# Performance work log

Hardware: AMD Instinct MI355X
Metric: run time of the kernel (lower is better)

## Reference

```python
import jax, jax.numpy as jnp
import numpy as np

N, E, F_IN, D, D_OUT = 100000, 1600000, 64, 20, 16
EPS = 1e-5


def _mean_agg(x, src, dst, n):
    # gather source features, scatter-mean onto destination nodes
    s = jax.ops.segment_sum(x[src], dst, num_segments=n)
    cnt = jax.ops.segment_sum(jnp.ones((src.shape[0], 1), x.dtype), dst, num_segments=n)
    return s / jnp.maximum(cnt, 1.0)


def _batchnorm(h, g, b):
    mu = jnp.mean(h, axis=0)
    var = jnp.mean(jnp.square(h - mu), axis=0)  # biased variance, BatchNorm1d training math
    return (h - mu) * jax.lax.rsqrt(var + EPS) * g + b


def _block(x, src, dst, Wl, bl, Wr, Ws, bs, Wn, bn, g, be):
    # SAGEConv: lin_l(mean_agg) + lin_r(x); plus linskip; then lin, BN, ReLU
    agg = _mean_agg(x, src, dst, N)
    h = agg @ Wl + bl + x @ Wr + x @ Ws + bs
    h = h @ Wn + bn
    return jax.nn.relu(_batchnorm(h, g, be))


def setup_inputs() -> dict:
    key = jax.random.key(0)
    ks = jax.random.split(key, 32)
    sc = lambda fi: 1.0 / np.sqrt(fi)
    d = {}
    d["x"] = jax.random.normal(ks[0], (N, F_IN), jnp.float32)
    d["edge_index"] = jax.random.randint(ks[1], (2, E), 0, N, dtype=jnp.int64)
    d["edge_attr"] = jax.random.normal(ks[2], (E, 1), jnp.float32)
    # layer 1 (in = F_IN)
    d["Wl1"] = jax.random.normal(ks[3], (F_IN, D), jnp.float32) * sc(F_IN)
    d["bl1"] = jnp.zeros((D,), jnp.float32)
    d["Wr1"] = jax.random.normal(ks[4], (F_IN, D), jnp.float32) * sc(F_IN)
    d["Ws1"] = jax.random.normal(ks[5], (F_IN, D), jnp.float32) * sc(F_IN)
    d["bs1"] = jnp.zeros((D,), jnp.float32)
    d["Wn1"] = jax.random.normal(ks[6], (D, D), jnp.float32) * sc(D)
    d["bn1"] = jnp.zeros((D,), jnp.float32)
    d["g1"] = jnp.ones((D,), jnp.float32)
    d["be1"] = jnp.zeros((D,), jnp.float32)
    # layers 2-4 stacked (in = D)
    d["Wlm"] = jax.random.normal(ks[7], (3, D, D), jnp.float32) * sc(D)
    d["blm"] = jnp.zeros((3, D), jnp.float32)
    d["Wrm"] = jax.random.normal(ks[8], (3, D, D), jnp.float32) * sc(D)
    d["Wsm"] = jax.random.normal(ks[9], (3, D, D), jnp.float32) * sc(D)
    d["bsm"] = jnp.zeros((3, D), jnp.float32)
    d["Wnm"] = jax.random.normal(ks[10], (3, D, D), jnp.float32) * sc(D)
    d["bnm"] = jnp.zeros((3, D), jnp.float32)
    d["gm"] = jnp.ones((3, D), jnp.float32)
    d["bem"] = jnp.zeros((3, D), jnp.float32)
    # layer 5 (no BN/ReLU, out = D_OUT)
    d["Wl5"] = jax.random.normal(ks[11], (D, D), jnp.float32) * sc(D)
    d["bl5"] = jnp.zeros((D,), jnp.float32)
    d["Wr5"] = jax.random.normal(ks[12], (D, D), jnp.float32) * sc(D)
    d["Ws5"] = jax.random.normal(ks[13], (D, D), jnp.float32) * sc(D)
    d["bs5"] = jnp.zeros((D,), jnp.float32)
    d["Wn5"] = jax.random.normal(ks[14], (D, D_OUT), jnp.float32) * sc(D)
    d["bn5"] = jnp.zeros((D_OUT,), jnp.float32)
    return d


def reference(x, edge_index, edge_attr,
              Wl1, bl1, Wr1, Ws1, bs1, Wn1, bn1, g1, be1,
              Wlm, blm, Wrm, Wsm, bsm, Wnm, bnm, gm, bem,
              Wl5, bl5, Wr5, Ws5, bs5, Wn5, bn5):
    src, dst = edge_index[0], edge_index[1]
    # edge_attr is accepted by the torch forward but unused
    h = _block(x, src, dst, Wl1, bl1, Wr1, Ws1, bs1, Wn1, bn1, g1, be1)
    for i in range(3):  # layers 2-4
        h = _block(h, src, dst, Wlm[i], blm[i], Wrm[i], Wsm[i], bsm[i],
                   Wnm[i], bnm[i], gm[i], bem[i])
    # layer 5: sage + skip, final linear, no norm/relu
    agg = _mean_agg(h, src, dst, N)
    h = agg @ Wl5 + bl5 + h @ Wr5 + h @ Ws5 + bs5
    return h @ Wn5 + bn5
```

## Files before the change

kernel.cpp:

```cpp
#include <hip/hip_runtime.h>

constexpr int Nn   = 100000;
constexpr int Ne   = 1600000;
constexpr int FINN = 64;
constexpr int Dh   = 20;
constexpr int Dout = 16;
constexpr float EPSV = 1e-5f;

constexpr int NR  = 16;
constexpr int RSZ = Nn / NR;
constexpr int NSL = 32;
constexpr int P1B = 400;
constexpr int P1E = Ne / P1B;

constexpr size_t OFF_WC1  = 0;
constexpr size_t OFF_C1   = 2560;
constexpr size_t OFF_WCM  = 2592;
constexpr size_t OFF_CM   = 4992;
constexpr size_t OFF_WC5  = 5088;
constexpr size_t OFF_C5   = 5728;
constexpr size_t OFF_ST   = 5760;
constexpr size_t OFF_OFFS = 8192;
constexpr size_t OFF_BSUM = 208896;
constexpr size_t OFF_CNT  = 209408;
constexpr size_t OFF_CSR  = 309760;
constexpr size_t OFF_XA   = 1910784;
constexpr size_t OFF_XB   = 3510784;
constexpr size_t OFF_HP   = 5110784;
constexpr size_t OFF_BHT  = OFF_HP;
constexpr size_t OFF_OBHT = OFF_HP + 6400;
constexpr size_t OFF_RB   = OFF_HP + 12800;

__device__ inline unsigned short f2b(float x) {
    unsigned b = __float_as_uint(x);
    return (unsigned short)((b + 0x7FFFu + ((b >> 16) & 1u)) >> 16);
}
__device__ inline float b2f(unsigned short u) {
    return __uint_as_float(((unsigned)u) << 16);
}
__device__ inline float blo(unsigned u) { return __uint_as_float(u << 16); }
__device__ inline float bhi(unsigned u) { return __uint_as_float(u & 0xFFFF0000u); }
__device__ inline unsigned bpack(float lo, float hi) {
    return (unsigned)f2b(lo) | ((unsigned)f2b(hi) << 16);
}

__global__ void prep_weights(
    const float* __restrict__ Wl1, const float* __restrict__ bl1,
    const float* __restrict__ Wr1, const float* __restrict__ Ws1,
    const float* __restrict__ bs1, const float* __restrict__ Wn1,
    const float* __restrict__ bn1,
    const float* __restrict__ Wlm, const float* __restrict__ blm,
    const float* __restrict__ Wrm, const float* __restrict__ Wsm,
    const float* __restrict__ bsm, const float* __restrict__ Wnm,
    const float* __restrict__ bnm,
    const float* __restrict__ Wl5, const float* __restrict__ bl5,
    const float* __restrict__ Wr5, const float* __restrict__ Ws5,
    const float* __restrict__ bs5, const float* __restrict__ Wn5,
    const float* __restrict__ bn5,
    float* __restrict__ wc1, float* __restrict__ c1,
    float* __restrict__ wcm, float* __restrict__ cm,
    float* __restrict__ wc5, float* __restrict__ c5)
{
    int layer = blockIdx.x;
    int t = threadIdx.x;
    if (layer == 0) {
        for (int idx = t; idx < FINN * Dh; idx += blockDim.x) {
            int k = idx / Dh, j = idx % Dh;
            float a = 0.f, b = 0.f;
            for (int d = 0; d < Dh; ++d) {
                float wn = Wn1[d * Dh + j];
                a += Wl1[k * Dh + d] * wn;
                b += (Wr1[k * Dh + d] + Ws1[k * Dh + d]) * wn;
            }
            wc1[k * 40 + j] = a;
            wc1[k * 40 + 20 + j] = b;
        }
        for (int j = t; j < Dh; j += blockDim.x) {
            float c0 = 0.f;
            for (int d = 0; d < Dh; ++d) c0 += (bl1[d] + bs1[d]) * Wn1[d * Dh + j];
            c1[j] = c0 + bn1[j];
        }
    } else if (layer <= 3) {
        int i = layer - 1;
        const float* Wl = Wlm + i * Dh * Dh;
        const float* Wr = Wrm + i * Dh * Dh;
        const float* Ws = Wsm + i * Dh * Dh;
        const float* Wn = Wnm + i * Dh * Dh;
        const float* bl = blm + i * Dh;
        const float* bs = bsm + i * Dh;
        const float* bn = bnm + i * Dh;
        float* wc = wcm + i * 800;
        float* cc = cm + i * 32;
        for (int idx = t; idx < Dh * Dh; idx += blockDim.x) {
            int k = idx / Dh, j = idx % Dh;
            float a = 0.f, b = 0.f;
            for (int d = 0; d < Dh; ++d) {
                float wn = Wn[d * Dh + j];
                a += Wl[k * Dh + d] * wn;
                b += (Wr[k * Dh + d] + Ws[k * Dh + d]) * wn;
            }
            wc[k * 40 + j] = a;
            wc[k * 40 + 20 + j] = b;
        }
        for (int j = t; j < Dh; j += blockDim.x) {
            float c0 = 0.f;
            for (int d = 0; d < Dh; ++d) c0 += (bl[d] + bs[d]) * Wn[d * Dh + j];
            cc[j] = c0 + bn[j];
        }
    } else {
        for (int idx = t; idx < Dh * Dout; idx += blockDim.x) {
            int k = idx / Dout, j = idx % Dout;
            float a = 0.f, b = 0.f;
            for (int d = 0; d < Dh; ++d) {
                float wn = Wn5[d * Dout + j];
                a += Wl5[k * Dh + d] * wn;
                b += (Wr5[k * Dh + d] + Ws5[k * Dh + d]) * wn;
            }
            wc5[k * 32 + j] = a;
            wc5[k * 32 + 16 + j] = b;
        }
        for (int j = t; j < Dout; j += blockDim.x) {
            float c0 = 0.f;
            for (int d = 0; d < Dh; ++d) c0 += (bl5[d] + bs5[d]) * Wn5[d * Dout + j];
            c5[j] = c0 + bn5[j];
        }
    }
}

__global__ __launch_bounds__(256) void hist1(const int* __restrict__ dst, unsigned* __restrict__ bhT) {
    __shared__ unsigned h[16 * NR];
    int b = blockIdx.x, t = threadIdx.x;
    for (int i = t; i < 16 * NR; i += 256) h[i] = 0;
    __syncthreads();
    int sub = t & 15;
    int e0 = b * P1E, e1 = min(e0 + P1E, Ne);
    for (int e = e0 + t; e < e1; e += 256) {
        int r = dst[e] / RSZ;
        atomicAdd(&h[sub * NR + r], 1u);
    }
    __syncthreads();
    if (t < NR) {
        unsigned s = 0;
        for (int i = 0; i < 16; ++i) s += h[i * NR + t];
        bhT[t * P1B + b] = s;
    }
}

__global__ __launch_bounds__(1024) void scan1(
    const unsigned* __restrict__ bhT, unsigned* __restrict__ obhT, unsigned* __restrict__ rbase)
{
    __shared__ unsigned rtot[NR];
    int t = threadIdx.x;
    int w = t >> 6, lane = t & 63;
    constexpr int PER = (P1B + 63) / 64;
    if (w < NR) {
        unsigned v[PER];
        unsigned s = 0;
#pragma unroll
        for (int i = 0; i < PER; ++i) {
            int b = lane * PER + i;
            v[i] = (b < P1B) ? bhT[w * P1B + b] : 0u;
            s += v[i];
        }
        unsigned val = s;
        for (int off = 1; off < 64; off <<= 1) {
            unsigned u = __shfl_up(val, off, 64);
            if (lane >= off) val += u;
        }
        unsigned run = val - s;
#pragma unroll
        for (int i = 0; i < PER; ++i) {
            int b = lane * PER + i;
            if (b < P1B) obhT[w * P1B + b] = run;
            run += v[i];
        }
        if (lane == 63) rtot[w] = val;
    }
    __syncthreads();
    if (t == 0) {
        unsigned base = 0;
        for (int r = 0; r < NR; ++r) { rbase[r] = base; base += rtot[r]; }
        rbase[NR] = base;
    }
}

__global__ __launch_bounds__(256) void scatter1(
    const int* __restrict__ src, const int* __restrict__ dst,
    const unsigned* __restrict__ obhT, const unsigned* __restrict__ rbase,
    unsigned* __restrict__ ebuf)
{
    __shared__ unsigned cur[NR];
    int b = blockIdx.x, t = threadIdx.x;
    if (t < NR) cur[t] = rbase[t] + obhT[t * P1B + b];
    __syncthreads();
    int e0 = b * P1E, e1 = min(e0 + P1E, Ne);
    for (int e = e0 + t; e < e1; e += 256) {
        int d = dst[e];
        int r = d / RSZ;
        unsigned dl = (unsigned)(d - r * RSZ);
        unsigned pos = atomicAdd(&cur[r], 1u);
        ebuf[pos] = (dl << 17) | (unsigned)src[e];
    }
}

__global__ __launch_bounds__(256) void hist2(
    const unsigned* __restrict__ ebuf, const unsigned* __restrict__ rbase,
    unsigned short* __restrict__ part)
{
    __shared__ unsigned h[RSZ];
    int b = blockIdx.x, t = threadIdx.x;
    int r = b % NR, s = b / NR;
    for (int i = t; i < RSZ; i += 256) h[i] = 0;
    __syncthreads();
    unsigned lo = rbase[r], hi = rbase[r + 1];
    unsigned step = (hi - lo + NSL - 1) / NSL;
    unsigned e0 = lo + (unsigned)s * step;
    unsigned e1 = e0 + step; if (e1 > hi) e1 = hi;
    for (unsigned e = e0 + t; e < e1; e += 256)
        atomicAdd(&h[ebuf[e] >> 17], 1u);
    __syncthreads();
    unsigned short* p = part + (size_t)b * RSZ;
    for (int i = t; i < RSZ; i += 256) p[i] = (unsigned short)h[i];
}

__global__ void col_prefix(unsigned short* __restrict__ part, unsigned* __restrict__ cnt) {
    int d = blockIdx.x * blockDim.x + threadIdx.x;
    if (d >= Nn) return;
    int r = d / RSZ, dl = d - r * RSZ;
    unsigned run = 0;
#pragma unroll
    for (int s = 0; s < NSL; ++s) {
        size_t idx = ((size_t)s * NR + r) * RSZ + dl;
        unsigned v = part[idx];
        part[idx] = (unsigned short)run;
        run += v;
    }
    cnt[d] = run;
}

__global__ void scan_blocksums(const unsigned* __restrict__ cnt, unsigned* __restrict__ bsum, int n) {
    __shared__ unsigned sd[256];
    int b = blockIdx.x, t = threadIdx.x;
    int base = b * 1024;
    unsigned s = 0;
    for (int i = t; i < 1024; i += 256) {
        int idx = base + i;
        if (idx < n) s += cnt[idx];
    }
    sd[t] = s;
    __syncthreads();
    for (int off = 128; off > 0; off >>= 1) {
        if (t < off) sd[t] += sd[t + off];
        __syncthreads();
    }
    if (t == 0) bsum[b] = sd[0];
}

__global__ void scan_bsum(unsigned* __restrict__ bsum, int nb) {
    __shared__ unsigned sh[128];
    int t = threadIdx.x;
    unsigned v = (t < nb) ? bsum[t] : 0u;
    sh[t] = v;
    __syncthreads();
    for (int off = 1; off < 128; off <<= 1) {
        unsigned add = (t >= off) ? sh[t - off] : 0u;
        __syncthreads();
        sh[t] += add;
        __syncthreads();
    }
    if (t < nb) bsum[t] = sh[t] - v;
}

__global__ void scan_final(const unsigned* __restrict__ cnt, const unsigned* __restrict__ bsum,
                           unsigned* __restrict__ offs, int n) {
    __shared__ unsigned wsum[4], woff[4];
    int b = blockIdx.x, t = threadIdx.x;
    int base = b * 1024 + t * 4;
    unsigned v[4];
    unsigned s = 0;
#pragma unroll
    for (int i = 0; i < 4; ++i) {
        int idx = base + i;
        v[i] = (idx < n) ? cnt[idx] : 0u;
        s += v[i];
    }
    unsigned lane = t & 63;
    int w = t >> 6;
    unsigned val = s;
    for (int off = 1; off < 64; off <<= 1) {
        unsigned u = __shfl_up(val, off, 64);
        if (lane >= off) val += u;
    }
    if (lane == 63) wsum[w] = val;
    __syncthreads();
    if (t == 0) {
        unsigned r = 0;
        for (int i = 0; i < 4; ++i) { woff[i] = r; r += wsum[i]; }
    }
    __syncthreads();
    unsigned run = bsum[b] + woff[w] + (val - s);
#pragma unroll
    for (int i = 0; i < 4; ++i) {
        int idx = base + i;
        if (idx < n) {
            offs[idx] = run;
            run += v[i];
            if (idx == n - 1) offs[n] = run;
        }
    }
}

__global__ __launch_bounds__(256) void fill2(
    const unsigned* __restrict__ ebuf, const unsigned* __restrict__ rbase,
    const unsigned* __restrict__ offs, const unsigned short* __restrict__ part,
    unsigned* __restrict__ csr)
{
    __shared__ unsigned cur[RSZ];
    int b = blockIdx.x, t = threadIdx.x;
    int r = b % NR, s = b / NR;
    int lon = r * RSZ;
    const unsigned short* p = part + (size_t)b * RSZ;
    for (int i = t; i < RSZ; i += 256)
        cur[i] = offs[lon + i] + p[i];
    __syncthreads();
    unsigned lo = rbase[r], hi = rbase[r + 1];
    unsigned step = (hi - lo + NSL - 1) / NSL;
    unsigned e0 = lo + (unsigned)s * step;
    unsigned e1 = e0 + step; if (e1 > hi) e1 = hi;
    for (unsigned e = e0 + t; e < e1; e += 256) {
        unsigned v = ebuf[e];
        unsigned pos = atomicAdd(&cur[v >> 17], 1u);
        csr[pos] = v & 0x1FFFFu;
    }
}

template <int FINt, int FO, bool NORM, bool INBF16>
__global__ __launch_bounds__(256) void gemm_kernel(
    const void* __restrict__ xin_, const float* __restrict__ stats,
    const float* __restrict__ g, const float* __restrict__ be,
    const float* __restrict__ wc, const float* __restrict__ cvec,
    unsigned short* __restrict__ xa, unsigned short* __restrict__ xb)
{
    constexpr int XS  = ((FO + 7) / 8) * 8;
    constexpr int XSI = ((FINt + 7) / 8) * 8;
    __shared__ float sscale[Dh], sshift[Dh];
    int t = threadIdx.x;
    if (NORM) {
        if (t < Dh) {
            float mu = stats[t] * (1.0f / Nn);
            float var = stats[32 + t] * (1.0f / Nn) - mu * mu;
            float sc = g[t] * rsqrtf(var + EPSV);
            sscale[t] = sc;
            sshift[t] = be[t] - mu * sc;
        }
        __syncthreads();
    }
    int n = blockIdx.x * blockDim.x + t;
    if (n >= Nn) return;

    float acc[2 * FO];
#pragma unroll
    for (int j = 0; j < 2 * FO; ++j) acc[j] = 0.f;

#pragma unroll
    for (int c = 0; c < FINt / 4; ++c) {
        float xs[4];
        if (INBF16) {
            const unsigned short* xr = (const unsigned short*)xin_ + (size_t)n * XSI;
            ushort4 v = *(const ushort4*)(xr + 4 * c);
            xs[0] = b2f(v.x); xs[1] = b2f(v.y); xs[2] = b2f(v.z); xs[3] = b2f(v.w);
        } else {
            const float* xr = (const float*)xin_ + (size_t)n * FINt;
            float4 v = *(const float4*)(xr + 4 * c);
            xs[0] = v.x; xs[1] = v.y; xs[2] = v.z; xs[3] = v.w;
        }
        if (NORM) {
#pragma unroll
            for (int kk = 0; kk < 4; ++kk)
                xs[kk] = fmaxf(xs[kk] * sscale[4 * c + kk] + sshift[4 * c + kk], 0.0f);
        }
#pragma unroll
        for (int kk = 0; kk < 4; ++kk) {
            float xk = xs[kk];
            const float* wr = wc + (4 * c + kk) * (2 * FO);
#pragma unroll
            for (int j = 0; j < 2 * FO; ++j) acc[j] = fmaf(xk, wr[j], acc[j]);
        }
    }

    unsigned short* xao = xa + (size_t)n * XS;
    unsigned short* xbo = xb + (size_t)n * XS;
#pragma unroll
    for (int c = 0; c < FO / 4; ++c) {
        ushort4 o;
        o.x = f2b(acc[4 * c + 0]);
        o.y = f2b(acc[4 * c + 1]);
        o.z = f2b(acc[4 * c + 2]);
        o.w = f2b(acc[4 * c + 3]);
        *(ushort4*)(xao + 4 * c) = o;
        ushort4 p;
        p.x = f2b(acc[FO + 4 * c + 0] + cvec[4 * c + 0]);
        p.y = f2b(acc[FO + 4 * c + 1] + cvec[4 * c + 1]);
        p.z = f2b(acc[FO + 4 * c + 2] + cvec[4 * c + 2]);
        p.w = f2b(acc[FO + 4 * c + 3] + cvec[4 * c + 3]);
        *(ushort4*)(xbo + 4 * c) = p;
    }
}

template <int F, bool WITH_STATS, bool OUTBF16>
__global__ __launch_bounds__(256) void pull_kernel(
    const unsigned* __restrict__ offs, const unsigned* __restrict__ csr,
    const unsigned short* __restrict__ xa, const unsigned short* __restrict__ xb,
    void* __restrict__ out_, float* __restrict__ stats)
{
    constexpr int C  = (F + 7) / 8;
    constexpr int XS = C * 8;
    __shared__ float sstat[2 * F];
    int t = threadIdx.x;
    if (WITH_STATS) {
        if (t < 2 * F) sstat[t] = 0.f;
        __syncthreads();
    }
    int tid = blockIdx.x * blockDim.x + t;
    int n = tid / C;
    int c = tid % C;
    int valid = (c == C - 1) ? (F - 8 * (C - 1)) : 8;
    bool act = (n < Nn);
    float h[8];
    if (act) {
        unsigned b = offs[n], e = offs[n + 1];
        const unsigned short* base = xa + c * 8;
        float acc[8];
#pragma unroll
        for (int j = 0; j < 8; ++j) acc[j] = 0.f;
        unsigned k = b;
        for (; k + 8 <= e; k += 8) {
            unsigned s[8];
#pragma unroll
            for (int i = 0; i < 8; ++i) s[i] = csr[k + i];
            uint4 v[8];
#pragma unroll
            for (int i = 0; i < 8; ++i) v[i] = *(const uint4*)(base + (size_t)s[i] * XS);
#pragma unroll
            for (int i = 0; i < 8; ++i) {
                acc[0] += blo(v[i].x); acc[1] += bhi(v[i].x);
                acc[2] += blo(v[i].y); acc[3] += bhi(v[i].y);
                acc[4] += blo(v[i].z); acc[5] += bhi(v[i].z);
                acc[6] += blo(v[i].w); acc[7] += bhi(v[i].w);
            }
        }
        for (; k < e; ++k) {
            unsigned s0 = csr[k];
            uint4 v = *(const uint4*)(base + (size_t)s0 * XS);
            acc[0] += blo(v.x); acc[1] += bhi(v.x);
            acc[2] += blo(v.y); acc[3] += bhi(v.y);
            acc[4] += blo(v.z); acc[5] += bhi(v.z);
            acc[6] += blo(v.w); acc[7] += bhi(v.w);
        }
        float inv = 1.0f / fmaxf((float)(e - b), 1.0f);
        uint4 xv = *(const uint4*)(xb + (size_t)n * XS + c * 8);
        float xf[8] = { blo(xv.x), bhi(xv.x), blo(xv.y), bhi(xv.y),
                        blo(xv.z), bhi(xv.z), blo(xv.w), bhi(xv.w) };
#pragma unroll
        for (int j = 0; j < 8; ++j) h[j] = fmaf(acc[j], inv, xf[j]);
        if (OUTBF16) {
            unsigned short* o = (unsigned short*)out_ + (size_t)n * XS + c * 8;
            if (valid == 8) {
                uint4 w;
                w.x = bpack(h[0], h[1]); w.y = bpack(h[2], h[3]);
                w.z = bpack(h[4], h[5]); w.w = bpack(h[6], h[7]);
                *(uint4*)o = w;
            } else {
                ushort4 w4;
                w4.x = f2b(h[0]); w4.y = f2b(h[1]); w4.z = f2b(h[2]); w4.w = f2b(h[3]);
                *(ushort4*)o = w4;
            }
        } else {
            float* o = (float*)out_ + (size_t)n * F + c * 8;
            float4 v0; v0.x = h[0]; v0.y = h[1]; v0.z = h[2]; v0.w = h[3];
            *(float4*)o = v0;
            if (valid == 8) {
                float4 v1; v1.x = h[4]; v1.y = h[5]; v1.z = h[6]; v1.w = h[7];
                *(float4*)(o + 4) = v1;
            }
        }
    }
    if (WITH_STATS) {
        if (act) {
            for (int j = 0; j < valid; ++j) {
                atomicAdd(&sstat[c * 8 + j], h[j]);
                atomicAdd(&sstat[F + c * 8 + j], h[j] * h[j]);
            }
        }
        __syncthreads();
        if (t < F) {
            atomicAdd(&stats[t], sstat[t]);
        } else if (t < 2 * F) {
            atomicAdd(&stats[32 + (t - F)], sstat[t]);
        }
    }
}

extern "C" void kernel_launch(void* const* d_in, const int* in_sizes, int n_in,
                              void* d_out, int out_size, void* d_ws, size_t ws_size,
                              hipStream_t stream) {
    const float* x   = (const float*)d_in[0];
    const int* ei    = (const int*)d_in[1];
    const int* esrc  = ei;
    const int* edst  = ei + Ne;
    const float* Wl1 = (const float*)d_in[3];
    const float* bl1 = (const float*)d_in[4];
    const float* Wr1 = (const float*)d_in[5];
    const float* Ws1 = (const float*)d_in[6];
    const float* bs1 = (const float*)d_in[7];
    const float* Wn1 = (const float*)d_in[8];
    const float* bn1 = (const float*)d_in[9];
    const float* g1  = (const float*)d_in[10];
    const float* be1 = (const float*)d_in[11];
    const float* Wlm = (const float*)d_in[12];
    const float* blm = (const float*)d_in[13];
    const float* Wrm = (const float*)d_in[14];
    const float* Wsm = (const float*)d_in[15];
    const float* bsm = (const float*)d_in[16];
    const float* Wnm = (const float*)d_in[17];
    const float* bnm = (const float*)d_in[18];
    const float* gm  = (const float*)d_in[19];
    const float* bem = (const float*)d_in[20];
    const float* Wl5 = (const float*)d_in[21];
    const float* bl5 = (const float*)d_in[22];
    const float* Wr5 = (const float*)d_in[23];
    const float* Ws5 = (const float*)d_in[24];
    const float* bs5 = (const float*)d_in[25];
    const float* Wn5 = (const float*)d_in[26];
    const float* bn5 = (const float*)d_in[27];

    float* ws   = (float*)d_ws;
    unsigned* u = (unsigned*)d_ws;
    float* wc1   = ws + OFF_WC1;
    float* c1    = ws + OFF_C1;
    float* wcm   = ws + OFF_WCM;
    float* cm    = ws + OFF_CM;
    float* wc5   = ws + OFF_WC5;
    float* c5    = ws + OFF_C5;
    float* stats = ws + OFF_ST;
    unsigned* offs = u + OFF_OFFS;
    unsigned* bsum = u + OFF_BSUM;
    unsigned* cnt  = u + OFF_CNT;
    unsigned* csr  = u + OFF_CSR;
    unsigned short* xa = (unsigned short*)(ws + OFF_XA);
    unsigned* ebuf = u + OFF_XA;
    unsigned short* xb = (unsigned short*)(ws + OFF_XB);
    unsigned short* part = (unsigned short*)(ws + OFF_XB);
    unsigned short* hp = (unsigned short*)(ws + OFF_HP);
    unsigned* bhT  = u + OFF_BHT;
    unsigned* obhT = u + OFF_OBHT;
    unsigned* rbase = u + OFF_RB;

    hipMemsetAsync(stats, 0, 256 * sizeof(float), stream);

    prep_weights<<<5, 256, 0, stream>>>(Wl1, bl1, Wr1, Ws1, bs1, Wn1, bn1,
                                        Wlm, blm, Wrm, Wsm, bsm, Wnm, bnm,
                                        Wl5, bl5, Wr5, Ws5, bs5, Wn5, bn5,
                                        wc1, c1, wcm, cm, wc5, c5);

    hist1<<<P1B, 256, 0, stream>>>(edst, bhT);
    scan1<<<1, 1024, 0, stream>>>(bhT, obhT, rbase);
    scatter1<<<P1B, 256, 0, stream>>>(esrc, edst, obhT, rbase, ebuf);
    hist2<<<NR * NSL, 256, 0, stream>>>(ebuf, rbase, part);
    col_prefix<<<(Nn + 255) / 256, 256, 0, stream>>>(part, cnt);
    constexpr int NB = (Nn + 1023) / 1024;
    scan_blocksums<<<NB, 256, 0, stream>>>(cnt, bsum, Nn);
    scan_bsum<<<1, 128, 0, stream>>>(bsum, NB);
    scan_final<<<NB, 256, 0, stream>>>(cnt, bsum, offs, Nn);
    fill2<<<NR * NSL, 256, 0, stream>>>(ebuf, rbase, offs, part, csr);

    int nblk = (Nn + 255) / 256;
    int pblk20 = (Nn * 3 + 255) / 256;
    int pblk16 = (Nn * 2 + 255) / 256;

    gemm_kernel<FINN, Dh, false, false><<<nblk, 256, 0, stream>>>(x, nullptr, nullptr, nullptr, wc1, c1, xa, xb);
    pull_kernel<Dh, true, true><<<pblk20, 256, 0, stream>>>(offs, csr, xa, xb, hp, stats + 0);
    gemm_kernel<Dh, Dh, true, true><<<nblk, 256, 0, stream>>>(hp, stats + 0, g1, be1, wcm + 0, cm + 0, xa, xb);
    pull_kernel<Dh, true, true><<<pblk20, 256, 0, stream>>>(offs, csr, xa, xb, hp, stats + 64);
    gemm_kernel<Dh, Dh, true, true><<<nblk, 256, 0, stream>>>(hp, stats + 64, gm + 0, bem + 0, wcm + 800, cm + 32, xa, xb);
    pull_kernel<Dh, true, true><<<pblk20, 256, 0, stream>>>(offs, csr, xa, xb, hp, stats + 128);
    gemm_kernel<Dh, Dh, true, true><<<nblk, 256, 0, stream>>>(hp, stats + 128, gm + 20, bem + 20, wcm + 1600, cm + 64, xa, xb);
    pull_kernel<Dh, true, true><<<pblk20, 256, 0, stream>>>(offs, csr, xa, xb, hp, stats + 192);
    gemm_kernel<Dh, Dout, true, true><<<nblk, 256, 0, stream>>>(hp, stats + 192, gm + 40, bem + 40, wc5, c5, xa, xb);
    pull_kernel<Dout, false, false><<<pblk16, 256, 0, stream>>>(offs, csr, xa, xb, d_out, nullptr);
}
```

Baseline: 403.2 us.

## Split per-node GEMM across threads per 8-column chunk with LDS weights

The per-node dense transform now assigns one thread per 8-output chunk of either the aggregate-side or root-side projection, instead of one thread computing all outputs for a node. Weights are staged in shared memory, and each thread writes one packed 16-byte bf16 store with padding zeroed. This raises parallelism and cuts per-thread registers, and the output stores become vectorised. In exchange, each input row is re-read by several threads, and there is extra work for the LDS weight load and index math.

```diff
diff --git a/kernel.cpp b/kernel.cpp
--- a/kernel.cpp
+++ b/kernel.cpp
@@ -343,8 +343,13 @@
 {
     constexpr int XS  = ((FO + 7) / 8) * 8;
     constexpr int XSI = ((FINt + 7) / 8) * 8;
+    constexpr int CH  = XS / 8;
+    constexpr int CL  = 2 * CH;
+    __shared__ float swl[FINt * 2 * FO + 8];
     __shared__ float sscale[Dh], sshift[Dh];
     int t = threadIdx.x;
+    for (int i = t; i < FINt * 2 * FO; i += 256) swl[i] = wc[i];
+    if (t < 8) swl[FINt * 2 * FO + t] = 0.f;
     if (NORM) {
         if (t < Dh) {
             float mu = stats[t] * (1.0f / Nn);
@@ -353,58 +358,61 @@
             sscale[t] = sc;
             sshift[t] = be[t] - mu * sc;
         }
-        __syncthreads();
-    }
-    int n = blockIdx.x * blockDim.x + t;
+    }
+    __syncthreads();
+    int tid = blockIdx.x * 256 + t;
+    int n = tid / CL;
+    int c = tid % CL;
     if (n >= Nn) return;
-
-    float acc[2 * FO];
-#pragma unroll
-    for (int j = 0; j < 2 * FO; ++j) acc[j] = 0.f;
-
-#pragma unroll
-    for (int c = 0; c < FINt / 4; ++c) {
+    int half = c / CH, cc = c % CH;
+    int off = half * FO + cc * 8;
+    int jmax = (cc == CH - 1) ? (FO - (CH - 1) * 8) : 8;
+
+    float acc[8];
+#pragma unroll
+    for (int j = 0; j < 8; ++j) acc[j] = 0.f;
+
+#pragma unroll
+    for (int k4 = 0; k4 < FINt / 4; ++k4) {
         float xs[4];
         if (INBF16) {
             const unsigned short* xr = (const unsigned short*)xin_ + (size_t)n * XSI;
-            ushort4 v = *(const ushort4*)(xr + 4 * c);
+            ushort4 v = *(const ushort4*)(xr + 4 * k4);
             xs[0] = b2f(v.x); xs[1] = b2f(v.y); xs[2] = b2f(v.z); xs[3] = b2f(v.w);
         } else {
             const float* xr = (const float*)xin_ + (size_t)n * FINt;
-            float4 v = *(const float4*)(xr + 4 * c);
+            float4 v = *(const float4*)(xr + 4 * k4);
             xs[0] = v.x; xs[1] = v.y; xs[2] = v.z; xs[3] = v.w;
         }
         if (NORM) {
 #pragma unroll
             for (int kk = 0; kk < 4; ++kk)
-                xs[kk] = fmaxf(xs[kk] * sscale[4 * c + kk] + sshift[4 * c + kk], 0.0f);
+                xs[kk] = fmaxf(xs[kk] * sscale[4 * k4 + kk] + sshift[4 * k4 + kk], 0.0f);
         }
 #pragma unroll
         for (int kk = 0; kk < 4; ++kk) {
             float xk = xs[kk];
-            const float* wr = wc + (4 * c + kk) * (2 * FO);
-#pragma unroll
-            for (int j = 0; j < 2 * FO; ++j) acc[j] = fmaf(xk, wr[j], acc[j]);
-        }
-    }
-
-    unsigned short* xao = xa + (size_t)n * XS;
-    unsigned short* xbo = xb + (size_t)n * XS;
-#pragma unroll
-    for (int c = 0; c < FO / 4; ++c) {
-        ushort4 o;
-        o.x = f2b(acc[4 * c + 0]);
-        o.y = f2b(acc[4 * c + 1]);
-        o.z = f2b(acc[4 * c + 2]);
-        o.w = f2b(acc[4 * c + 3]);
-        *(ushort4*)(xao + 4 * c) = o;
-        ushort4 p;
-        p.x = f2b(acc[FO + 4 * c + 0] + cvec[4 * c + 0]);
-        p.y = f2b(acc[FO + 4 * c + 1] + cvec[4 * c + 1]);
-        p.z = f2b(acc[FO + 4 * c + 2] + cvec[4 * c + 2]);
-        p.w = f2b(acc[FO + 4 * c + 3] + cvec[4 * c + 3]);
-        *(ushort4*)(xbo + 4 * c) = p;
-    }
+            const float* wr = &swl[(4 * k4 + kk) * (2 * FO) + off];
+#pragma unroll
+            for (int j = 0; j < 8; ++j) acc[j] = fmaf(xk, wr[j], acc[j]);
+        }
+    }
+
+    float hv[8];
+#pragma unroll
+    for (int j = 0; j < 8; ++j) hv[j] = acc[j];
+    if (half) {
+#pragma unroll
+        for (int j = 0; j < 8; ++j) hv[j] += cvec[cc * 8 + j];
+    }
+#pragma unroll
+    for (int j = 0; j < 8; ++j) if (j >= jmax) hv[j] = 0.f;
+
+    unsigned short* dstp = (half ? xb : xa) + (size_t)n * XS + cc * 8;
+    uint4 w;
+    w.x = bpack(hv[0], hv[1]); w.y = bpack(hv[2], hv[3]);
+    w.z = bpack(hv[4], hv[5]); w.w = bpack(hv[6], hv[7]);
+    *(uint4*)dstp = w;
 }
 
 template <int F, bool WITH_STATS, bool OUTBF16>
@@ -574,18 +582,19 @@
     scan_final<<<NB, 256, 0, stream>>>(cnt, bsum, offs, Nn);
     fill2<<<NR * NSL, 256, 0, stream>>>(ebuf, rbase, offs, part, csr);
 
-    int nblk = (Nn + 255) / 256;
+    int gblk20 = (Nn * 6 + 255) / 256;
+    int gblk16 = (Nn * 4 + 255) / 256;
     int pblk20 = (Nn * 3 + 255) / 256;
     int pblk16 = (Nn * 2 + 255) / 256;
 
-    gemm_kernel<FINN, Dh, false, false><<<nblk, 256, 0, stream>>>(x, nullptr, nullptr, nullptr, wc1, c1, xa, xb);
+    gemm_kernel<FINN, Dh, false, false><<<gblk20, 256, 0, stream>>>(x, nullptr, nullptr, nullptr, wc1, c1, xa, xb);
     pull_kernel<Dh, true, true><<<pblk20, 256, 0, stream>>>(offs, csr, xa, xb, hp, stats + 0);
-    gemm_kernel<Dh, Dh, true, true><<<nblk, 256, 0, stream>>>(hp, stats + 0, g1, be1, wcm + 0, cm + 0, xa, xb);
+    gemm_kernel<Dh, Dh, true, true><<<gblk20, 256, 0, stream>>>(hp, stats + 0, g1, be1, wcm + 0, cm + 0, xa, xb);
     pull_kernel<Dh, true, true><<<pblk20, 256, 0, stream>>>(offs, csr, xa, xb, hp, stats + 64);
-    gemm_kernel<Dh, Dh, true, true><<<nblk, 256, 0, stream>>>(hp, stats + 64, gm + 0, bem + 0, wcm + 800, cm + 32, xa, xb);
+    gemm_kernel<Dh, Dh, true, true><<<gblk20, 256, 0, stream>>>(hp, stats + 64, gm + 0, bem + 0, wcm + 800, cm + 32, xa, xb);
     pull_kernel<Dh, true, true><<<pblk20, 256, 0, stream>>>(offs, csr, xa, xb, hp, stats + 128);
-    gemm_kernel<Dh, Dh, true, true><<<nblk, 256, 0, stream>>>(hp, stats + 128, gm + 20, bem + 20, wcm + 1600, cm + 64, xa, xb);
+    gemm_kernel<Dh, Dh, true, true><<<gblk20, 256, 0, stream>>>(hp, stats + 128, gm + 20, bem + 20, wcm + 1600, cm + 64, xa, xb);
     pull_kernel<Dh, true, true><<<pblk20, 256, 0, stream>>>(offs, csr, xa, xb, hp, stats + 192);
-    gemm_kernel<Dh, Dout, true, true><<<nblk, 256, 0, stream>>>(hp, stats + 192, gm + 40, bem + 40, wc5, c5, xa, xb);
+    gemm_kernel<Dh, Dout, true, true><<<gblk16, 256, 0, stream>>>(hp, stats + 192, gm + 40, bem + 40, wc5, c5, xa, xb);
     pull_kernel<Dout, false, false><<<pblk16, 256, 0, stream>>>(offs, csr, xa, xb, d_out, nullptr);
 }
```

New measurement: 352.4 us. 12.6% less time.
